# Performance work log

Measured on AMD Instinct MI355X. Metric: run time of the kernel, lower is better.

The kernel has to match this reference:

```python
import jax, jax.numpy as jnp
import numpy as np

BN_EPS = 1e-5


def lstm_scan(x, Wih, Whh, b):
    # x: [B, T, I] -> outputs [B, T, H]; PyTorch gate order i, f, g, o
    B = x.shape[0]
    H = Whh.shape[1]
    xs = jnp.swapaxes(x, 0, 1)  # [T, B, I]

    def step(carry, xt):
        h, c = carry
        z = xt @ Wih.T + h @ Whh.T + b  # [B, 4H]
        i, f, g, o = jnp.split(z, 4, axis=-1)
        c = jax.nn.sigmoid(f) * c + jax.nn.sigmoid(i) * jnp.tanh(g)
        h = jax.nn.sigmoid(o) * jnp.tanh(c)
        return (h, c), h

    init = (jnp.zeros((B, H), x.dtype), jnp.zeros((B, H), x.dtype))
    _, hs = jax.lax.scan(step, init, xs)
    return jnp.swapaxes(hs, 0, 1)


def bilstm(x, Wf, Uf, bf, Wr, Ur, br):
    fwd = lstm_scan(x, Wf, Uf, bf)
    rev = lstm_scan(x[:, ::-1], Wr, Ur, br)[:, ::-1]
    return jnp.concatenate([fwd, rev], axis=-1)


def batchnorm(x, g, b):
    # training-mode BN: batch mean, biased variance (PyTorch forward default)
    mu = x.mean(axis=0)
    var = x.var(axis=0)
    return g * (x - mu) * jax.lax.rsqrt(var + BN_EPS) + b


def setup_inputs() -> dict:
    key = jax.random.key(0)
    ks = jax.random.split(key, 20)
    B = 1048576
    idx = jax.random.randint(ks[0], (B, 1), 0, 8).astype(jnp.float32)
    feats = jax.random.normal(ks[1], (B, 7), dtype=jnp.float32)
    x = jnp.concatenate([idx, feats], axis=1)  # [B, 8]

    def p(k, shape):
        return 0.1 * jax.random.normal(k, shape, dtype=jnp.float32)

    return {
        "x": x,
        "emb": p(ks[2], (8, 2)),
        "W1": p(ks[3], (18, 9)), "b1": p(ks[4], (18,)),
        "g1": jnp.ones((18,), jnp.float32), "be1": jnp.zeros((18,), jnp.float32),
        "W2": p(ks[5], (9, 18)), "b2": p(ks[6], (9,)),
        "g2": jnp.ones((9,), jnp.float32), "be2": jnp.zeros((9,), jnp.float32),
        # lstm1: input 1, hidden 2, bidirectional
        "l1Wf": p(ks[7], (8, 1)), "l1Uf": p(ks[8], (8, 2)), "l1bf": p(ks[9], (8,)),
        "l1Wr": p(ks[10], (8, 1)), "l1Ur": p(ks[11], (8, 2)), "l1br": p(ks[12], (8,)),
        # lstm2: input 4, hidden 1, bidirectional
        "l2Wf": p(ks[13], (4, 4)), "l2Uf": p(ks[14], (4, 1)), "l2bf": p(ks[15], (4,)),
        "l2Wr": p(ks[16], (4, 4)), "l2Ur": p(ks[17], (4, 1)), "l2br": p(ks[18], (4,)),
    }


def reference(x, emb, W1, b1, g1, be1, W2, b2, g2, be2,
              l1Wf, l1Uf, l1bf, l1Wr, l1Ur, l1br,
              l2Wf, l2Uf, l2bf, l2Wr, l2Ur, l2br):
    idx = x[:, 0].astype(jnp.int32)
    e = emb[idx]                                   # [B, 2]
    h = jnp.concatenate([e, x[:, 1:]], axis=1)     # [B, 9]
    h = jax.nn.relu(batchnorm(h @ W1.T + b1, g1, be1))   # [B, 18]
    h = jax.nn.relu(batchnorm(h @ W2.T + b2, g2, be2))   # [B, 9]
    h = h[:, :, None]                              # [B, 9, 1]
    h = jax.nn.relu(bilstm(h, l1Wf, l1Uf, l1bf, l1Wr, l1Ur, l1br))  # [B, 9, 4]
    h = bilstm(h, l2Wf, l2Uf, l2bf, l2Wr, l2Ur, l2br)               # [B, 9, 2]
    return h.reshape(-1, 9, 2)
```

## Files before the change

kernel.cpp:

```cpp
#include <hip/hip_runtime.h>

#define LOG2E 1.4426950408889634f
#define BN_EPS 1e-5f

typedef float f32x2 __attribute__((ext_vector_type(2)));
typedef float f32x4 __attribute__((ext_vector_type(4)));

__device__ __forceinline__ float sigf(float x){
    return __builtin_amdgcn_rcpf(1.f + __builtin_amdgcn_exp2f(-LOG2E * x));
}
__device__ __forceinline__ float sigtanh(float a, float b){
    float A  = __builtin_amdgcn_exp2f(LOG2E * a);
    float Bv = __builtin_amdgcn_exp2f((2.f * LOG2E) * b);
    float num = A * (Bv - 1.f);
    float den = (1.f + A) * (1.f + Bv);
    return num * __builtin_amdgcn_rcpf(den);
}
__device__ __forceinline__ float relu_(float x){ return fmaxf(x, 0.f); }

__device__ __forceinline__ float wsum(float v){
    #pragma unroll
    for (int m = 32; m >= 1; m >>= 1) v += __shfl_xor(v, m, 64);
    return v;
}

__device__ constexpr int TRI(int j, int l){ return j*9 - j*(j-1)/2 + (l - j); }

__device__ __forceinline__ void load_h0(const float* __restrict__ x, const float* __restrict__ emb,
                                        long row, float h0[9])
{
    const float4* xv = (const float4*)(x + row * 8);
    float4 p = xv[0];
    float4 q = xv[1];
    int idx = (int)p.x;
    float2 e = ((const float2*)emb)[idx];
    h0[0] = e.x; h0[1] = e.y;
    h0[2] = p.y; h0[3] = p.z; h0[4] = p.w;
    h0[5] = q.x; h0[6] = q.y; h0[7] = q.z; h0[8] = q.w;
}

__global__ __launch_bounds__(256) void k_moments(const float* __restrict__ x, const float* __restrict__ emb,
                                                 float* __restrict__ stats, int B)
{
    float s9[9], mt[45];
    #pragma unroll
    for (int j = 0; j < 9; ++j) s9[j] = 0.f;
    #pragma unroll
    for (int t = 0; t < 45; ++t) mt[t] = 0.f;

    long base = (long)blockIdx.x * 1024 + threadIdx.x;
    #pragma unroll
    for (int r = 0; r < 4; ++r){
        long row = base + r * 256;
        if (row < B){
            float h0[9];
            load_h0(x, emb, row, h0);
            #pragma unroll
            for (int j = 0; j < 9; ++j){
                s9[j] += h0[j];
                #pragma unroll
                for (int l = j; l < 9; ++l)
                    mt[TRI(j,l)] = fmaf(h0[j], h0[l], mt[TRI(j,l)]);
            }
        }
    }
    __shared__ float sm[54];
    if (threadIdx.x < 54) sm[threadIdx.x] = 0.f;
    __syncthreads();
    bool l0 = (threadIdx.x & 63) == 0;
    #pragma unroll
    for (int j = 0; j < 9; ++j){
        float v = wsum(s9[j]);
        if (l0) atomicAdd(&sm[j], v);
    }
    #pragma unroll
    for (int t = 0; t < 45; ++t){
        float v = wsum(mt[t]);
        if (l0) atomicAdd(&sm[9 + t], v);
    }
    __syncthreads();
    if (threadIdx.x < 9)  atomicAdd(&stats[threadIdx.x], sm[threadIdx.x]);
    else if (threadIdx.x < 54) atomicAdd(&stats[16 + threadIdx.x - 9], sm[threadIdx.x]);
}

__device__ __forceinline__ void bn1_from_moments(const float* __restrict__ stats,
                                                 const float* __restrict__ W1, const float* __restrict__ b1,
                                                 const float* __restrict__ g1, const float* __restrict__ be1,
                                                 float invB, float* smem_sc, float* smem_sh)
{
    if (threadIdx.x < 18){
        int k = threadIdx.x;
        float w[9];
        #pragma unroll
        for (int j = 0; j < 9; ++j) w[j] = W1[k*9 + j];
        float dot9 = 0.f, q = 0.f;
        #pragma unroll
        for (int j = 0; j < 9; ++j){
            dot9 = fmaf(w[j], stats[j], dot9);
            q = fmaf(w[j]*w[j], stats[16 + TRI(j,j)], q);
            #pragma unroll
            for (int l = j+1; l < 9; ++l)
                q = fmaf(2.f*w[j]*w[l], stats[16 + TRI(j,l)], q);
        }
        float m1  = dot9 * invB;
        float var = fmaf(-m1, m1, q * invB);
        float mu  = m1 + b1[k];
        float sc  = g1[k] * __builtin_amdgcn_rsqf(var + BN_EPS);
        smem_sc[k] = sc;
        smem_sh[k] = fmaf(-mu, sc, be1[k]);
    }
    __syncthreads();
}

template<int STORE_Z2>
__global__ __launch_bounds__(256) void k_stats2(const float* __restrict__ x, const float* __restrict__ emb,
                                                const float* __restrict__ W1, const float* __restrict__ b1,
                                                const float* __restrict__ g1, const float* __restrict__ be1,
                                                const float* __restrict__ W2, const float* __restrict__ b2,
                                                float* __restrict__ stats, float* __restrict__ z2buf, int B)
{
    __shared__ float s_sc[18], s_sh[18];
    bn1_from_moments(stats, W1, b1, g1, be1, 1.f/(float)B, s_sc, s_sh);

    float sc1[18], sh1[18];
    #pragma unroll
    for (int k = 0; k < 18; ++k){ sc1[k] = s_sc[k]; sh1[k] = s_sh[k]; }

    float as[9], aq[9];
    #pragma unroll
    for (int k = 0; k < 9; ++k){ as[k] = 0.f; aq[k] = 0.f; }

    long base = (long)blockIdx.x * 1024 + threadIdx.x;
    #pragma unroll
    for (int r = 0; r < 4; ++r){
        long row = base + r * 256;
        if (row < B){
            float h0[9];
            load_h0(x, emb, row, h0);
            float a1[18];
            #pragma unroll
            for (int k = 0; k < 18; ++k){
                float s = b1[k];
                #pragma unroll
                for (int j = 0; j < 9; ++j) s = fmaf(W1[k*9 + j], h0[j], s);
                a1[k] = relu_(fmaf(sc1[k], s, sh1[k]));
            }
            #pragma unroll
            for (int k = 0; k < 9; ++k){
                float s = b2[k];
                #pragma unroll
                for (int j = 0; j < 18; ++j) s = fmaf(W2[k*18 + j], a1[j], s);
                as[k] += s; aq[k] = fmaf(s, s, aq[k]);
                if (STORE_Z2) z2buf[(long)k * B + row] = s;
            }
        }
    }
    __shared__ float sm[18];
    if (threadIdx.x < 18) sm[threadIdx.x] = 0.f;
    __syncthreads();
    bool l0 = (threadIdx.x & 63) == 0;
    #pragma unroll
    for (int k = 0; k < 9; ++k){
        float s = wsum(as[k]);
        float q = wsum(aq[k]);
        if (l0){ atomicAdd(&sm[k], s); atomicAdd(&sm[9 + k], q); }
    }
    __syncthreads();
    if (threadIdx.x < 9)       atomicAdd(&stats[64 + threadIdx.x], sm[threadIdx.x]);
    else if (threadIdx.x < 18) atomicAdd(&stats[80 + threadIdx.x - 9], sm[threadIdx.x]);
}

__device__ __forceinline__ f32x2 mk2(float a, float b){ f32x2 r; r.x=a; r.y=b; return r; }
__device__ __forceinline__ f32x4 mk4(float a, float b, float c, float d){ f32x4 r; r.x=a; r.y=b; r.z=c; r.w=d; return r; }

template<int USE_WS>
__global__ __launch_bounds__(256) void k_main(const float* __restrict__ x, const float* __restrict__ emb,
    const float* __restrict__ W1, const float* __restrict__ b1,
    const float* __restrict__ g1, const float* __restrict__ be1,
    const float* __restrict__ W2, const float* __restrict__ b2,
    const float* __restrict__ g2, const float* __restrict__ be2,
    const float* __restrict__ w1f, const float* __restrict__ u1f, const float* __restrict__ c1f,
    const float* __restrict__ w1r, const float* __restrict__ u1r, const float* __restrict__ c1r,
    const float* __restrict__ w2f, const float* __restrict__ u2f, const float* __restrict__ c2f,
    const float* __restrict__ w2r, const float* __restrict__ u2r, const float* __restrict__ c2r,
    const float* __restrict__ stats, const float* __restrict__ z2buf,
    float* __restrict__ out, int B)
{
    __shared__ float s_sc[18], s_sh[18];
    float invB = 1.f / (float)B;
    if (!USE_WS) bn1_from_moments(stats, W1, b1, g1, be1, invB, s_sc, s_sh);

    long row = (long)blockIdx.x * 256 + threadIdx.x;
    if (row >= B) return;

    float a2[9];
    #pragma unroll
    for (int k = 0; k < 9; ++k){
        float zc;
        if (USE_WS){
            zc = z2buf[(long)k * B + row];
        } else {
            zc = 0.f;
        }
        a2[k] = zc;
    }
    if (!USE_WS){
        float h0[9];
        load_h0(x, emb, row, h0);
        float a1[18];
        #pragma unroll
        for (int k = 0; k < 18; ++k){
            float s = b1[k];
            #pragma unroll
            for (int j = 0; j < 9; ++j) s = fmaf(W1[k*9 + j], h0[j], s);
            a1[k] = relu_(fmaf(s_sc[k], s, s_sh[k]));
        }
        #pragma unroll
        for (int k = 0; k < 9; ++k){
            float s = b2[k];
            #pragma unroll
            for (int j = 0; j < 18; ++j) s = fmaf(W2[k*18 + j], a1[j], s);
            a2[k] = s;
        }
    }
    #pragma unroll
    for (int k = 0; k < 9; ++k){
        float mu  = stats[64 + k] * invB;
        float var = fmaf(-mu, mu, stats[80 + k] * invB);
        float sc  = g2[k] * __builtin_amdgcn_rsqf(var + BN_EPS);
        a2[k] = relu_(fmaf(sc, a2[k] - mu, be2[k]));
    }

    f32x4 W4[4], U04[4], U14[4], B4[4];
    #pragma unroll
    for (int g = 0; g < 4; ++g){
        W4[g]  = mk4(w1f[2*g], w1f[2*g+1], w1r[2*g], w1r[2*g+1]);
        U04[g] = mk4(u1f[(2*g)*2], u1f[(2*g+1)*2], u1r[(2*g)*2], u1r[(2*g+1)*2]);
        U14[g] = mk4(u1f[(2*g)*2+1], u1f[(2*g+1)*2+1], u1r[(2*g)*2+1], u1r[(2*g+1)*2+1]);
        B4[g]  = mk4(c1f[2*g], c1f[2*g+1], c1r[2*g], c1r[2*g+1]);
    }
    f32x4 h4 = {0.f, 0.f, 0.f, 0.f};
    f32x4 c4 = {0.f, 0.f, 0.f, 0.f};
    float u_[9][4];
    #pragma unroll
    for (int s = 0; s < 9; ++s){
        const int tf = s, tr = 8 - s;
        f32x4 xt4 = mk4(a2[tf], a2[tf], a2[tr], a2[tr]);
        f32x4 hx  = mk4(h4.x, h4.x, h4.z, h4.z);
        f32x4 hy  = mk4(h4.y, h4.y, h4.w, h4.w);
        f32x4 z[4];
        #pragma unroll
        for (int g = 0; g < 4; ++g)
            z[g] = __builtin_elementwise_fma(W4[g], xt4,
                    __builtin_elementwise_fma(U04[g], hx,
                     __builtin_elementwise_fma(U14[g], hy, B4[g])));
        f32x4 icg, fs;
        #pragma unroll
        for (int c = 0; c < 4; ++c){
            icg[c] = sigtanh(z[0][c], z[2][c]);
            fs[c]  = sigf(z[1][c]);
        }
        c4 = __builtin_elementwise_fma(fs, c4, icg);
        #pragma unroll
        for (int c = 0; c < 4; ++c) h4[c] = sigtanh(z[3][c], c4[c]);
        u_[tf][0] = relu_(h4.x);
        u_[tf][1] = relu_(h4.y);
        u_[tr][2] = relu_(h4.z);
        u_[tr][3] = relu_(h4.w);
    }

    f32x2 w2v[4][4], u2v[4], b2v[4];
    #pragma unroll
    for (int r = 0; r < 4; ++r){
        #pragma unroll
        for (int j = 0; j < 4; ++j) w2v[r][j] = mk2(w2f[4*r + j], w2r[4*r + j]);
        u2v[r] = mk2(u2f[r], u2r[r]);
        b2v[r] = mk2(c2f[r], c2r[r]);
    }
    f32x2 h2 = {0.f, 0.f};
    f32x2 cc = {0.f, 0.f};
    long obase = row * 18;
    #pragma unroll
    for (int s = 0; s < 9; ++s){
        const int tf = s, tr = 8 - s;
        f32x2 z[4];
        #pragma unroll
        for (int r = 0; r < 4; ++r){
            f32x2 acc = __builtin_elementwise_fma(u2v[r], h2, b2v[r]);
            #pragma unroll
            for (int j = 0; j < 4; ++j)
                acc = __builtin_elementwise_fma(w2v[r][j], mk2(u_[tf][j], u_[tr][j]), acc);
            z[r] = acc;
        }
        f32x2 icg, fs;
        #pragma unroll
        for (int c = 0; c < 2; ++c){
            icg[c] = sigtanh(z[0][c], z[2][c]);
            fs[c]  = sigf(z[1][c]);
        }
        cc = __builtin_elementwise_fma(fs, cc, icg);
        float hfo = sigtanh(z[3][0], cc.x);
        float hro = sigtanh(z[3][1], cc.y);
        h2 = mk2(hfo, hro);
        out[obase + 2*tf]     = hfo;
        out[obase + 2*tr + 1] = hro;
    }
}

extern "C" void kernel_launch(void* const* d_in, const int* in_sizes, int n_in,
                              void* d_out, int out_size, void* d_ws, size_t ws_size,
                              hipStream_t stream)
{
    const float* x    = (const float*)d_in[0];
    const float* emb  = (const float*)d_in[1];
    const float* W1   = (const float*)d_in[2];
    const float* b1   = (const float*)d_in[3];
    const float* g1   = (const float*)d_in[4];
    const float* be1  = (const float*)d_in[5];
    const float* W2   = (const float*)d_in[6];
    const float* b2   = (const float*)d_in[7];
    const float* g2   = (const float*)d_in[8];
    const float* be2  = (const float*)d_in[9];
    const float* l1Wf = (const float*)d_in[10];
    const float* l1Uf = (const float*)d_in[11];
    const float* l1bf = (const float*)d_in[12];
    const float* l1Wr = (const float*)d_in[13];
    const float* l1Ur = (const float*)d_in[14];
    const float* l1br = (const float*)d_in[15];
    const float* l2Wf = (const float*)d_in[16];
    const float* l2Uf = (const float*)d_in[17];
    const float* l2bf = (const float*)d_in[18];
    const float* l2Wr = (const float*)d_in[19];
    const float* l2Ur = (const float*)d_in[20];
    const float* l2br = (const float*)d_in[21];

    int B = in_sizes[0] / 8;
    float* stats = (float*)d_ws;
    float* z2buf = (float*)d_ws + 1024;
    size_t need = (1024 + (size_t)9 * B) * sizeof(float);
    bool use_ws = ws_size >= need;

    hipMemsetAsync(d_ws, 0, 128 * sizeof(float), stream);

    int nb12 = (B + 1023) / 1024;
    int nb3  = (B + 255) / 256;

    k_moments<<<nb12, 256, 0, stream>>>(x, emb, stats, B);
    if (use_ws){
        k_stats2<1><<<nb12, 256, 0, stream>>>(x, emb, W1, b1, g1, be1, W2, b2, stats, z2buf, B);
        k_main<1><<<nb3, 256, 0, stream>>>(x, emb, W1, b1, g1, be1, W2, b2, g2, be2,
                                           l1Wf, l1Uf, l1bf, l1Wr, l1Ur, l1br,
                                           l2Wf, l2Uf, l2bf, l2Wr, l2Ur, l2br,
                                           stats, z2buf, (float*)d_out, B);
    } else {
        k_stats2<0><<<nb12, 256, 0, stream>>>(x, emb, W1, b1, g1, be1, W2, b2, stats, z2buf, B);
        k_main<0><<<nb3, 256, 0, stream>>>(x, emb, W1, b1, g1, be1, W2, b2, g2, be2,
                                           l1Wf, l1Uf, l1bf, l1Wr, l1Ur, l1br,
                                           l2Wf, l2Uf, l2bf, l2Wr, l2Ur, l2br,
                                           stats, z2buf, (float*)d_out, B);
    }
}
```

Measured before the change: 152.9 us.

## Fuse three passes into one cooperative kernel with grid syncs, keeping z2 in registers

Replaces the moments, stats2 and main kernels with a single cooperative kernel that uses grid.sync between the BN statistics phases. Each thread keeps its four rows' z2 values in registers, which removes the 9*B workspace write and re-read and the extra kernel launches. Outputs are staged and written as float2 pairs. The cost is that all 1024 blocks must be co-resident (launch_bounds 256,4), which means high register pressure and possible spills. If the occupancy check fails, the code falls back to a three-kernel path that recomputes z2.

```diff
diff --git a/kernel.cpp b/kernel.cpp
--- a/kernel.cpp
+++ b/kernel.cpp
@@ -1,4 +1,7 @@
 #include <hip/hip_runtime.h>
+#include <hip/hip_cooperative_groups.h>
+
+namespace cg = cooperative_groups;
 
 #define LOG2E 1.4426950408889634f
 #define BN_EPS 1e-5f
@@ -39,50 +42,6 @@
     h0[5] = q.x; h0[6] = q.y; h0[7] = q.z; h0[8] = q.w;
 }
 
-__global__ __launch_bounds__(256) void k_moments(const float* __restrict__ x, const float* __restrict__ emb,
-                                                 float* __restrict__ stats, int B)
-{
-    float s9[9], mt[45];
-    #pragma unroll
-    for (int j = 0; j < 9; ++j) s9[j] = 0.f;
-    #pragma unroll
-    for (int t = 0; t < 45; ++t) mt[t] = 0.f;
-
-    long base = (long)blockIdx.x * 1024 + threadIdx.x;
-    #pragma unroll
-    for (int r = 0; r < 4; ++r){
-        long row = base + r * 256;
-        if (row < B){
-            float h0[9];
-            load_h0(x, emb, row, h0);
-            #pragma unroll
-            for (int j = 0; j < 9; ++j){
-                s9[j] += h0[j];
-                #pragma unroll
-                for (int l = j; l < 9; ++l)
-                    mt[TRI(j,l)] = fmaf(h0[j], h0[l], mt[TRI(j,l)]);
-            }
-        }
-    }
-    __shared__ float sm[54];
-    if (threadIdx.x < 54) sm[threadIdx.x] = 0.f;
-    __syncthreads();
-    bool l0 = (threadIdx.x & 63) == 0;
-    #pragma unroll
-    for (int j = 0; j < 9; ++j){
-        float v = wsum(s9[j]);
-        if (l0) atomicAdd(&sm[j], v);
-    }
-    #pragma unroll
-    for (int t = 0; t < 45; ++t){
-        float v = wsum(mt[t]);
-        if (l0) atomicAdd(&sm[9 + t], v);
-    }
-    __syncthreads();
-    if (threadIdx.x < 9)  atomicAdd(&stats[threadIdx.x], sm[threadIdx.x]);
-    else if (threadIdx.x < 54) atomicAdd(&stats[16 + threadIdx.x - 9], sm[threadIdx.x]);
-}
-
 __device__ __forceinline__ void bn1_from_moments(const float* __restrict__ stats,
                                                  const float* __restrict__ W1, const float* __restrict__ b1,
                                                  const float* __restrict__ g1, const float* __restrict__ be1,
@@ -112,23 +71,233 @@
     __syncthreads();
 }
 
-template<int STORE_Z2>
-__global__ __launch_bounds__(256) void k_stats2(const float* __restrict__ x, const float* __restrict__ emb,
-                                                const float* __restrict__ W1, const float* __restrict__ b1,
-                                                const float* __restrict__ g1, const float* __restrict__ be1,
-                                                const float* __restrict__ W2, const float* __restrict__ b2,
-                                                float* __restrict__ stats, float* __restrict__ z2buf, int B)
-{
-    __shared__ float s_sc[18], s_sh[18];
-    bn1_from_moments(stats, W1, b1, g1, be1, 1.f/(float)B, s_sc, s_sh);
-
-    float sc1[18], sh1[18];
-    #pragma unroll
-    for (int k = 0; k < 18; ++k){ sc1[k] = s_sc[k]; sh1[k] = s_sh[k]; }
-
-    float as[9], aq[9];
-    #pragma unroll
-    for (int k = 0; k < 9; ++k){ as[k] = 0.f; aq[k] = 0.f; }
+__device__ __forceinline__ f32x2 mk2(float a, float b){ f32x2 r; r.x=a; r.y=b; return r; }
+__device__ __forceinline__ f32x4 mk4(float a, float b, float c, float d){ f32x4 r; r.x=a; r.y=b; r.z=c; r.w=d; return r; }
+
+struct KParams {
+    const float *x, *emb, *W1, *b1, *g1, *be1, *W2, *b2, *g2, *be2;
+    const float *w1f, *u1f, *c1f, *w1r, *u1r, *c1r;
+    const float *w2f, *u2f, *c2f, *w2r, *u2r, *c2r;
+    float* stats;
+    float* out;
+    int B;
+};
+
+__global__ __launch_bounds__(256, 4) void k_fused(KParams p)
+{
+    cg::grid_group grid = cg::this_grid();
+    const int tid = threadIdx.x;
+    const long base = (long)blockIdx.x * 1024 + tid;
+    const float invB = 1.f / (float)p.B;
+    const bool l0 = (tid & 63) == 0;
+
+    {
+        float s9[9], mt[45];
+        #pragma unroll
+        for (int j = 0; j < 9; ++j) s9[j] = 0.f;
+        #pragma unroll
+        for (int t = 0; t < 45; ++t) mt[t] = 0.f;
+
+        #pragma unroll
+        for (int r = 0; r < 4; ++r){
+            long row = base + r * 256;
+            if (row < p.B){
+                float h0[9];
+                load_h0(p.x, p.emb, row, h0);
+                #pragma unroll
+                for (int j = 0; j < 9; ++j){
+                    s9[j] += h0[j];
+                    #pragma unroll
+                    for (int l = j; l < 9; ++l)
+                        mt[TRI(j,l)] = fmaf(h0[j], h0[l], mt[TRI(j,l)]);
+                }
+            }
+        }
+        __shared__ float sm[54];
+        if (tid < 54) sm[tid] = 0.f;
+        __syncthreads();
+        #pragma unroll
+        for (int j = 0; j < 9; ++j){
+            float v = wsum(s9[j]);
+            if (l0) atomicAdd(&sm[j], v);
+        }
+        #pragma unroll
+        for (int t = 0; t < 45; ++t){
+            float v = wsum(mt[t]);
+            if (l0) atomicAdd(&sm[9 + t], v);
+        }
+        __syncthreads();
+        if (tid < 9)       atomicAdd(&p.stats[tid], sm[tid]);
+        else if (tid < 54) atomicAdd(&p.stats[16 + tid - 9], sm[tid]);
+    }
+
+    grid.sync();
+
+    float z2r[4][9];
+    {
+        __shared__ float s_sc[18], s_sh[18];
+        bn1_from_moments(p.stats, p.W1, p.b1, p.g1, p.be1, invB, s_sc, s_sh);
+
+        float sc1[18], sh1[18];
+        #pragma unroll
+        for (int k = 0; k < 18; ++k){ sc1[k] = s_sc[k]; sh1[k] = s_sh[k]; }
+
+        float as[9], aq[9];
+        #pragma unroll
+        for (int k = 0; k < 9; ++k){ as[k] = 0.f; aq[k] = 0.f; }
+
+        #pragma unroll
+        for (int r = 0; r < 4; ++r){
+            long row = base + r * 256;
+            if (row < p.B){
+                float h0[9];
+                load_h0(p.x, p.emb, row, h0);
+                float a1[18];
+                #pragma unroll
+                for (int k = 0; k < 18; ++k){
+                    float s = p.b1[k];
+                    #pragma unroll
+                    for (int j = 0; j < 9; ++j) s = fmaf(p.W1[k*9 + j], h0[j], s);
+                    a1[k] = relu_(fmaf(sc1[k], s, sh1[k]));
+                }
+                #pragma unroll
+                for (int k = 0; k < 9; ++k){
+                    float s = p.b2[k];
+                    #pragma unroll
+                    for (int j = 0; j < 18; ++j) s = fmaf(p.W2[k*18 + j], a1[j], s);
+                    z2r[r][k] = s;
+                    as[k] += s; aq[k] = fmaf(s, s, aq[k]);
+                }
+            } else {
+                #pragma unroll
+                for (int k = 0; k < 9; ++k) z2r[r][k] = 0.f;
+            }
+        }
+        __shared__ float sm2[18];
+        if (tid < 18) sm2[tid] = 0.f;
+        __syncthreads();
+        #pragma unroll
+        for (int k = 0; k < 9; ++k){
+            float s = wsum(as[k]);
+            float q = wsum(aq[k]);
+            if (l0){ atomicAdd(&sm2[k], s); atomicAdd(&sm2[9 + k], q); }
+        }
+        __syncthreads();
+        if (tid < 9)       atomicAdd(&p.stats[64 + tid], sm2[tid]);
+        else if (tid < 18) atomicAdd(&p.stats[80 + tid - 9], sm2[tid]);
+    }
+
+    grid.sync();
+
+    float sc2[9], sh2[9];
+    #pragma unroll
+    for (int k = 0; k < 9; ++k){
+        float mu  = p.stats[64 + k] * invB;
+        float var = fmaf(-mu, mu, p.stats[80 + k] * invB);
+        float sc  = p.g2[k] * __builtin_amdgcn_rsqf(var + BN_EPS);
+        sc2[k] = sc;
+        sh2[k] = fmaf(-mu, sc, p.be2[k]);
+    }
+
+    f32x4 W4[4], U04[4], U14[4], B4[4];
+    #pragma unroll
+    for (int g = 0; g < 4; ++g){
+        W4[g]  = mk4(p.w1f[2*g], p.w1f[2*g+1], p.w1r[2*g], p.w1r[2*g+1]);
+        U04[g] = mk4(p.u1f[(2*g)*2], p.u1f[(2*g+1)*2], p.u1r[(2*g)*2], p.u1r[(2*g+1)*2]);
+        U14[g] = mk4(p.u1f[(2*g)*2+1], p.u1f[(2*g+1)*2+1], p.u1r[(2*g)*2+1], p.u1r[(2*g+1)*2+1]);
+        B4[g]  = mk4(p.c1f[2*g], p.c1f[2*g+1], p.c1r[2*g], p.c1r[2*g+1]);
+    }
+    f32x2 w2v[4][4], u2v[4], b2v[4];
+    #pragma unroll
+    for (int r = 0; r < 4; ++r){
+        #pragma unroll
+        for (int j = 0; j < 4; ++j) w2v[r][j] = mk2(p.w2f[4*r + j], p.w2r[4*r + j]);
+        u2v[r] = mk2(p.u2f[r], p.u2r[r]);
+        b2v[r] = mk2(p.c2f[r], p.c2r[r]);
+    }
+
+    #pragma unroll
+    for (int r = 0; r < 4; ++r){
+        long row = base + r * 256;
+        if (row >= p.B) continue;
+
+        float a2[9];
+        #pragma unroll
+        for (int k = 0; k < 9; ++k)
+            a2[k] = relu_(fmaf(sc2[k], z2r[r][k], sh2[k]));
+
+        f32x4 h4 = {0.f, 0.f, 0.f, 0.f};
+        f32x4 c4 = {0.f, 0.f, 0.f, 0.f};
+        float u_[9][4];
+        #pragma unroll
+        for (int s = 0; s < 9; ++s){
+            const int tf = s, tr = 8 - s;
+            f32x4 xt4 = mk4(a2[tf], a2[tf], a2[tr], a2[tr]);
+            f32x4 hx  = mk4(h4.x, h4.x, h4.z, h4.z);
+            f32x4 hy  = mk4(h4.y, h4.y, h4.w, h4.w);
+            f32x4 z[4];
+            #pragma unroll
+            for (int g = 0; g < 4; ++g)
+                z[g] = __builtin_elementwise_fma(W4[g], xt4,
+                        __builtin_elementwise_fma(U04[g], hx,
+                         __builtin_elementwise_fma(U14[g], hy, B4[g])));
+            f32x4 icg, fs;
+            #pragma unroll
+            for (int c = 0; c < 4; ++c){
+                icg[c] = sigtanh(z[0][c], z[2][c]);
+                fs[c]  = sigf(z[1][c]);
+            }
+            c4 = __builtin_elementwise_fma(fs, c4, icg);
+            #pragma unroll
+            for (int c = 0; c < 4; ++c) h4[c] = sigtanh(z[3][c], c4[c]);
+            u_[tf][0] = relu_(h4.x);
+            u_[tf][1] = relu_(h4.y);
+            u_[tr][2] = relu_(h4.z);
+            u_[tr][3] = relu_(h4.w);
+        }
+
+        f32x2 h2 = {0.f, 0.f};
+        f32x2 cc = {0.f, 0.f};
+        float of[9], orr[9];
+        #pragma unroll
+        for (int s = 0; s < 9; ++s){
+            const int tf = s, tr = 8 - s;
+            f32x2 z[4];
+            #pragma unroll
+            for (int g = 0; g < 4; ++g){
+                f32x2 acc = __builtin_elementwise_fma(u2v[g], h2, b2v[g]);
+                #pragma unroll
+                for (int j = 0; j < 4; ++j)
+                    acc = __builtin_elementwise_fma(w2v[g][j], mk2(u_[tf][j], u_[tr][j]), acc);
+                z[g] = acc;
+            }
+            f32x2 icg, fs;
+            #pragma unroll
+            for (int c = 0; c < 2; ++c){
+                icg[c] = sigtanh(z[0][c], z[2][c]);
+                fs[c]  = sigf(z[1][c]);
+            }
+            cc = __builtin_elementwise_fma(fs, cc, icg);
+            float hfo = sigtanh(z[3][0], cc.x);
+            float hro = sigtanh(z[3][1], cc.y);
+            h2 = mk2(hfo, hro);
+            of[tf]  = hfo;
+            orr[tr] = hro;
+        }
+        float2* op = (float2*)(p.out + row * 18);
+        #pragma unroll
+        for (int t = 0; t < 9; ++t) op[t] = make_float2(of[t], orr[t]);
+    }
+}
+
+__global__ __launch_bounds__(256) void k_moments(const float* __restrict__ x, const float* __restrict__ emb,
+                                                 float* __restrict__ stats, int B)
+{
+    float s9[9], mt[45];
+    #pragma unroll
+    for (int j = 0; j < 9; ++j) s9[j] = 0.f;
+    #pragma unroll
+    for (int t = 0; t < 45; ++t) mt[t] = 0.f;
 
     long base = (long)blockIdx.x * 1024 + threadIdx.x;
     #pragma unroll
@@ -137,21 +306,68 @@
         if (row < B){
             float h0[9];
             load_h0(x, emb, row, h0);
+            #pragma unroll
+            for (int j = 0; j < 9; ++j){
+                s9[j] += h0[j];
+                #pragma unroll
+                for (int l = j; l < 9; ++l)
+                    mt[TRI(j,l)] = fmaf(h0[j], h0[l], mt[TRI(j,l)]);
+            }
+        }
+    }
+    __shared__ float sm[54];
+    if (threadIdx.x < 54) sm[threadIdx.x] = 0.f;
+    __syncthreads();
+    bool l0 = (threadIdx.x & 63) == 0;
+    #pragma unroll
+    for (int j = 0; j < 9; ++j){
+        float v = wsum(s9[j]);
+        if (l0) atomicAdd(&sm[j], v);
+    }
+    #pragma unroll
+    for (int t = 0; t < 45; ++t){
+        float v = wsum(mt[t]);
+        if (l0) atomicAdd(&sm[9 + t], v);
+    }
+    __syncthreads();
+    if (threadIdx.x < 9)  atomicAdd(&stats[threadIdx.x], sm[threadIdx.x]);
+    else if (threadIdx.x < 54) atomicAdd(&stats[16 + threadIdx.x - 9], sm[threadIdx.x]);
+}
+
+__global__ __launch_bounds__(256) void k_stats2(KParams p)
+{
+    __shared__ float s_sc[18], s_sh[18];
+    bn1_from_moments(p.stats, p.W1, p.b1, p.g1, p.be1, 1.f/(float)p.B, s_sc, s_sh);
+
+    float sc1[18], sh1[18];
+    #pragma unroll
+    for (int k = 0; k < 18; ++k){ sc1[k] = s_sc[k]; sh1[k] = s_sh[k]; }
+
+    float as[9], aq[9];
+    #pragma unroll
+    for (int k = 0; k < 9; ++k){ as[k] = 0.f; aq[k] = 0.f; }
+
+    long base = (long)blockIdx.x * 1024 + threadIdx.x;
+    #pragma unroll
+    for (int r = 0; r < 4; ++r){
+        long row = base + r * 256;
+        if (row < p.B){
+            float h0[9];
+            load_h0(p.x, p.emb, row, h0);
             float a1[18];
             #pragma unroll
             for (int k = 0; k < 18; ++k){
-                float s = b1[k];
-                #pragma unroll
-                for (int j = 0; j < 9; ++j) s = fmaf(W1[k*9 + j], h0[j], s);
+                float s = p.b1[k];
+                #pragma unroll
+                for (int j = 0; j < 9; ++j) s = fmaf(p.W1[k*9 + j], h0[j], s);
                 a1[k] = relu_(fmaf(sc1[k], s, sh1[k]));
             }
             #pragma unroll
             for (int k = 0; k < 9; ++k){
-                float s = b2[k];
-                #pragma unroll
-                for (int j = 0; j < 18; ++j) s = fmaf(W2[k*18 + j], a1[j], s);
+                float s = p.b2[k];
+                #pragma unroll
+                for (int j = 0; j < 18; ++j) s = fmaf(p.W2[k*18 + j], a1[j], s);
                 as[k] += s; aq[k] = fmaf(s, s, aq[k]);
-                if (STORE_Z2) z2buf[(long)k * B + row] = s;
             }
         }
     }
@@ -166,78 +382,48 @@
         if (l0){ atomicAdd(&sm[k], s); atomicAdd(&sm[9 + k], q); }
     }
     __syncthreads();
-    if (threadIdx.x < 9)       atomicAdd(&stats[64 + threadIdx.x], sm[threadIdx.x]);
-    else if (threadIdx.x < 18) atomicAdd(&stats[80 + threadIdx.x - 9], sm[threadIdx.x]);
-}
-
-__device__ __forceinline__ f32x2 mk2(float a, float b){ f32x2 r; r.x=a; r.y=b; return r; }
-__device__ __forceinline__ f32x4 mk4(float a, float b, float c, float d){ f32x4 r; r.x=a; r.y=b; r.z=c; r.w=d; return r; }
-
-template<int USE_WS>
-__global__ __launch_bounds__(256) void k_main(const float* __restrict__ x, const float* __restrict__ emb,
-    const float* __restrict__ W1, const float* __restrict__ b1,
-    const float* __restrict__ g1, const float* __restrict__ be1,
-    const float* __restrict__ W2, const float* __restrict__ b2,
-    const float* __restrict__ g2, const float* __restrict__ be2,
-    const float* __restrict__ w1f, const float* __restrict__ u1f, const float* __restrict__ c1f,
-    const float* __restrict__ w1r, const float* __restrict__ u1r, const float* __restrict__ c1r,
-    const float* __restrict__ w2f, const float* __restrict__ u2f, const float* __restrict__ c2f,
-    const float* __restrict__ w2r, const float* __restrict__ u2r, const float* __restrict__ c2r,
-    const float* __restrict__ stats, const float* __restrict__ z2buf,
-    float* __restrict__ out, int B)
+    if (threadIdx.x < 9)       atomicAdd(&p.stats[64 + threadIdx.x], sm[threadIdx.x]);
+    else if (threadIdx.x < 18) atomicAdd(&p.stats[80 + threadIdx.x - 9], sm[threadIdx.x]);
+}
+
+__global__ __launch_bounds__(256) void k_main_fb(KParams p)
 {
     __shared__ float s_sc[18], s_sh[18];
-    float invB = 1.f / (float)B;
-    if (!USE_WS) bn1_from_moments(stats, W1, b1, g1, be1, invB, s_sc, s_sh);
+    float invB = 1.f / (float)p.B;
+    bn1_from_moments(p.stats, p.W1, p.b1, p.g1, p.be1, invB, s_sc, s_sh);
 
     long row = (long)blockIdx.x * 256 + threadIdx.x;
-    if (row >= B) return;
-
+    if (row >= p.B) return;
+
+    float h0[9];
+    load_h0(p.x, p.emb, row, h0);
+    float a1[18];
+    #pragma unroll
+    for (int k = 0; k < 18; ++k){
+        float s = p.b1[k];
+        #pragma unroll
+        for (int j = 0; j < 9; ++j) s = fmaf(p.W1[k*9 + j], h0[j], s);
+        a1[k] = relu_(fmaf(s_sc[k], s, s_sh[k]));
+    }
     float a2[9];
     #pragma unroll
     for (int k = 0; k < 9; ++k){
-        float zc;
-        if (USE_WS){
-            zc = z2buf[(long)k * B + row];
-        } else {
-            zc = 0.f;
-        }
-        a2[k] = zc;
-    }
-    if (!USE_WS){
-        float h0[9];
-        load_h0(x, emb, row, h0);
-        float a1[18];
-        #pragma unroll
-        for (int k = 0; k < 18; ++k){
-            float s = b1[k];
-            #pragma unroll
-            for (int j = 0; j < 9; ++j) s = fmaf(W1[k*9 + j], h0[j], s);
-            a1[k] = relu_(fmaf(s_sc[k], s, s_sh[k]));
-        }
-        #pragma unroll
-        for (int k = 0; k < 9; ++k){
-            float s = b2[k];
-            #pragma unroll
-            for (int j = 0; j < 18; ++j) s = fmaf(W2[k*18 + j], a1[j], s);
-            a2[k] = s;
-        }
-    }
-    #pragma unroll
-    for (int k = 0; k < 9; ++k){
-        float mu  = stats[64 + k] * invB;
-        float var = fmaf(-mu, mu, stats[80 + k] * invB);
-        float sc  = g2[k] * __builtin_amdgcn_rsqf(var + BN_EPS);
-        a2[k] = relu_(fmaf(sc, a2[k] - mu, be2[k]));
+        float s = p.b2[k];
+        #pragma unroll
+        for (int j = 0; j < 18; ++j) s = fmaf(p.W2[k*18 + j], a1[j], s);
+        float mu  = p.stats[64 + k] * invB;
+        float var = fmaf(-mu, mu, p.stats[80 + k] * invB);
+        float sc  = p.g2[k] * __builtin_amdgcn_rsqf(var + BN_EPS);
+        a2[k] = relu_(fmaf(sc, s - mu, p.be2[k]));
     }
 
     f32x4 W4[4], U04[4], U14[4], B4[4];
     #pragma unroll
     for (int g = 0; g < 4; ++g){
-        W4[g]  = mk4(w1f[2*g], w1f[2*g+1], w1r[2*g], w1r[2*g+1]);
-        U04[g] = mk4(u1f[(2*g)*2], u1f[(2*g+1)*2], u1r[(2*g)*2], u1r[(2*g+1)*2]);
-        U14[g] = mk4(u1f[(2*g)*2+1], u1f[(2*g+1)*2+1], u1r[(2*g)*2+1], u1r[(2*g+1)*2+1]);
-        B4[g]  = mk4(c1f[2*g], c1f[2*g+1], c1r[2*g], c1r[2*g+1]);
+        W4[g]  = mk4(p.w1f[2*g], p.w1f[2*g+1], p.w1r[2*g], p.w1r[2*g+1]);
+        U04[g] = mk4(p.u1f[(2*g)*2], p.u1f[(2*g+1)*2], p.u1r[(2*g)*2], p.u1r[(2*g+1)*2]);
+        U14[g] = mk4(p.u1f[(2*g)*2+1], p.u1f[(2*g+1)*2+1], p.u1r[(2*g)*2+1], p.u1r[(2*g+1)*2+1]);
+        B4[g]  = mk4(p.c1f[2*g], p.c1f[2*g+1], p.c1r[2*g], p.c1r[2*g+1]);
     }
     f32x4 h4 = {0.f, 0.f, 0.f, 0.f};
     f32x4 c4 = {0.f, 0.f, 0.f, 0.f};
@@ -273,24 +459,24 @@
     #pragma unroll
     for (int r = 0; r < 4; ++r){
         #pragma unroll
-        for (int j = 0; j < 4; ++j) w2v[r][j] = mk2(w2f[4*r + j], w2r[4*r + j]);
-        u2v[r] = mk2(u2f[r], u2r[r]);
-        b2v[r] = mk2(c2f[r], c2r[r]);
+        for (int j = 0; j < 4; ++j) w2v[r][j] = mk2(p.w2f[4*r + j], p.w2r[4*r + j]);
+        u2v[r] = mk2(p.u2f[r], p.u2r[r]);
+        b2v[r] = mk2(p.c2f[r], p.c2r[r]);
     }
     f32x2 h2 = {0.f, 0.f};
     f32x2 cc = {0.f, 0.f};
-    long obase = row * 18;
+    float of[9], orr[9];
     #pragma unroll
     for (int s = 0; s < 9; ++s){
         const int tf = s, tr = 8 - s;
         f32x2 z[4];
         #pragma unroll
-        for (int r = 0; r < 4; ++r){
-            f32x2 acc = __builtin_elementwise_fma(u2v[r], h2, b2v[r]);
+        for (int g = 0; g < 4; ++g){
+            f32x2 acc = __builtin_elementwise_fma(u2v[g], h2, b2v[g]);
             #pragma unroll
             for (int j = 0; j < 4; ++j)
-                acc = __builtin_elementwise_fma(w2v[r][j], mk2(u_[tf][j], u_[tr][j]), acc);
-            z[r] = acc;
+                acc = __builtin_elementwise_fma(w2v[g][j], mk2(u_[tf][j], u_[tr][j]), acc);
+            z[g] = acc;
         }
         f32x2 icg, fs;
         #pragma unroll
@@ -302,61 +488,66 @@
         float hfo = sigtanh(z[3][0], cc.x);
         float hro = sigtanh(z[3][1], cc.y);
         h2 = mk2(hfo, hro);
-        out[obase + 2*tf]     = hfo;
-        out[obase + 2*tr + 1] = hro;
-    }
+        of[tf]  = hfo;
+        orr[tr] = hro;
+    }
+    float2* op = (float2*)(p.out + row * 18);
+    #pragma unroll
+    for (int t = 0; t < 9; ++t) op[t] = make_float2(of[t], orr[t]);
 }
 
 extern "C" void kernel_launch(void* const* d_in, const int* in_sizes, int n_in,
                               void* d_out, int out_size, void* d_ws, size_t ws_size,
                               hipStream_t stream)
 {
-    const float* x    = (const float*)d_in[0];
-    const float* emb  = (const float*)d_in[1];
-    const float* W1   = (const float*)d_in[2];
-    const float* b1   = (const float*)d_in[3];
-    const float* g1   = (const float*)d_in[4];
-    const float* be1  = (const float*)d_in[5];
-    const float* W2   = (const float*)d_in[6];
-    const float* b2   = (const float*)d_in[7];
-    const float* g2   = (const float*)d_in[8];
-    const float* be2  = (const float*)d_in[9];
-    const float* l1Wf = (const float*)d_in[10];
-    const float* l1Uf = (const float*)d_in[11];
-    const float* l1bf = (const float*)d_in[12];
-    const float* l1Wr = (const float*)d_in[13];
-    const float* l1Ur = (const float*)d_in[14];
-    const float* l1br = (const float*)d_in[15];
-    const float* l2Wf = (const float*)d_in[16];
-    const float* l2Uf = (const float*)d_in[17];
-    const float* l2bf = (const float*)d_in[18];
-    const float* l2Wr = (const float*)d_in[19];
-    const float* l2Ur = (const float*)d_in[20];
-    const float* l2br = (const float*)d_in[21];
-
-    int B = in_sizes[0] / 8;
-    float* stats = (float*)d_ws;
-    float* z2buf = (float*)d_ws + 1024;
-    size_t need = (1024 + (size_t)9 * B) * sizeof(float);
-    bool use_ws = ws_size >= need;
+    KParams p;
+    p.x    = (const float*)d_in[0];
+    p.emb  = (const float*)d_in[1];
+    p.W1   = (const float*)d_in[2];
+    p.b1   = (const float*)d_in[3];
+    p.g1   = (const float*)d_in[4];
+    p.be1  = (const float*)d_in[5];
+    p.W2   = (const float*)d_in[6];
+    p.b2   = (const float*)d_in[7];
+    p.g2   = (const float*)d_in[8];
+    p.be2  = (const float*)d_in[9];
+    p.w1f  = (const float*)d_in[10];
+    p.u1f  = (const float*)d_in[11];
+    p.c1f  = (const float*)d_in[12];
+    p.w1r  = (const float*)d_in[13];
+    p.u1r  = (const float*)d_in[14];
+    p.c1r  = (const float*)d_in[15];
+    p.w2f  = (const float*)d_in[16];
+    p.u2f  = (const float*)d_in[17];
+    p.c2f  = (const float*)d_in[18];
+    p.w2r  = (const float*)d_in[19];
+    p.u2r  = (const float*)d_in[20];
+    p.c2r  = (const float*)d_in[21];
+    p.stats = (float*)d_ws;
+    p.out   = (float*)d_out;
+    p.B     = in_sizes[0] / 8;
 
     hipMemsetAsync(d_ws, 0, 128 * sizeof(float), stream);
 
-    int nb12 = (B + 1023) / 1024;
-    int nb3  = (B + 255) / 256;
-
-    k_moments<<<nb12, 256, 0, stream>>>(x, emb, stats, B);
-    if (use_ws){
-        k_stats2<1><<<nb12, 256, 0, stream>>>(x, emb, W1, b1, g1, be1, W2, b2, stats, z2buf, B);
-        k_main<1><<<nb3, 256, 0, stream>>>(x, emb, W1, b1, g1, be1, W2, b2, g2, be2,
-                                           l1Wf, l1Uf, l1bf, l1Wr, l1Ur, l1br,
-                                           l2Wf, l2Uf, l2bf, l2Wr, l2Ur, l2br,
-                                           stats, z2buf, (float*)d_out, B);
-    } else {
-        k_stats2<0><<<nb12, 256, 0, stream>>>(x, emb, W1, b1, g1, be1, W2, b2, stats, z2buf, B);
-        k_main<0><<<nb3, 256, 0, stream>>>(x, emb, W1, b1, g1, be1, W2, b2, g2, be2,
-                                           l1Wf, l1Uf, l1bf, l1Wr, l1Ur, l1br,
-                                           l2Wf, l2Uf, l2bf, l2Wr, l2Ur, l2br,
-                                           stats, z2buf, (float*)d_out, B);
-    }
-}
+    int nb = (p.B + 1023) / 1024;
+
+    bool coop_done = false;
+    int dev = 0;
+    hipGetDevice(&dev);
+    int cus = 0;
+    hipDeviceGetAttribute(&cus, hipDeviceAttributeMultiprocessorCount, dev);
+    int maxb = 0;
+    hipError_t oe = hipOccupancyMaxActiveBlocksPerMultiprocessor(&maxb, k_fused, 256, 0);
+    if (oe == hipSuccess && cus > 0 && (long)maxb * cus >= nb){
+        void* args[] = { (void*)&p };
+        hipError_t e = hipLaunchCooperativeKernel((void*)k_fused, dim3(nb), dim3(256), args, 0, stream);
+        coop_done = (e == hipSuccess);
+    }
+
+    if (!coop_done){
+        int nb3 = (p.B + 255) / 256;
+        k_moments<<<nb, 256, 0, stream>>>(p.x, p.emb, p.stats, p.B);
+        k_stats2<<<nb, 256, 0, stream>>>(p);
+        k_main_fb<<<nb3, 256, 0, stream>>>(p);
+    }
+}
```

New measurement: 155.4 us. No clear change (+1.6%).

## Process two rows per thread with packed f32x2 math across rows

Applied to the files above, without the earlier changes.

The main kernel now has each thread handle two batch rows (rA and rA+256) and packs the two rows into f32x2 lanes. Before, the forward and reverse directions were packed into f32x4. All LSTM gate FMAs and activations run on these two-row vectors, so uniform weights broadcast as scalars and packed FMA can be used. The grid is halved. This raises per-thread ILP and amortizes weight loads, but increases register pressure and reduces the number of waves in flight.

```diff
diff --git a/kernel.cpp b/kernel.cpp
--- a/kernel.cpp
+++ b/kernel.cpp
@@ -4,18 +4,7 @@
 #define BN_EPS 1e-5f
 
 typedef float f32x2 __attribute__((ext_vector_type(2)));
-typedef float f32x4 __attribute__((ext_vector_type(4)));
-
-__device__ __forceinline__ float sigf(float x){
-    return __builtin_amdgcn_rcpf(1.f + __builtin_amdgcn_exp2f(-LOG2E * x));
-}
-__device__ __forceinline__ float sigtanh(float a, float b){
-    float A  = __builtin_amdgcn_exp2f(LOG2E * a);
-    float Bv = __builtin_amdgcn_exp2f((2.f * LOG2E) * b);
-    float num = A * (Bv - 1.f);
-    float den = (1.f + A) * (1.f + Bv);
-    return num * __builtin_amdgcn_rcpf(den);
-}
+
 __device__ __forceinline__ float relu_(float x){ return fmaxf(x, 0.f); }
 
 __device__ __forceinline__ float wsum(float v){
@@ -171,10 +160,34 @@
 }
 
 __device__ __forceinline__ f32x2 mk2(float a, float b){ f32x2 r; r.x=a; r.y=b; return r; }
-__device__ __forceinline__ f32x4 mk4(float a, float b, float c, float d){ f32x4 r; r.x=a; r.y=b; r.z=c; r.w=d; return r; }
+__device__ __forceinline__ f32x2 sp2(float a){ f32x2 r; r.x=a; r.y=a; return r; }
+__device__ __forceinline__ f32x2 exp2v(f32x2 v){
+    f32x2 r; r.x = __builtin_amdgcn_exp2f(v.x); r.y = __builtin_amdgcn_exp2f(v.y); return r;
+}
+__device__ __forceinline__ f32x2 rcpv(f32x2 v){
+    f32x2 r; r.x = __builtin_amdgcn_rcpf(v.x); r.y = __builtin_amdgcn_rcpf(v.y); return r;
+}
+__device__ __forceinline__ f32x2 relu2(f32x2 v){
+    f32x2 r; r.x = fmaxf(v.x, 0.f); r.y = fmaxf(v.y, 0.f); return r;
+}
+__device__ __forceinline__ f32x2 fmas(float a, f32x2 b, f32x2 c){
+    return __builtin_elementwise_fma(sp2(a), b, c);
+}
+
+__device__ __forceinline__ f32x2 cellh2(f32x2 zi, f32x2 zf, f32x2 zg, f32x2 zo, f32x2& c){
+    f32x2 A  = exp2v(sp2(LOG2E) * zi);
+    f32x2 G  = exp2v(sp2(2.f*LOG2E) * zg);
+    f32x2 icg = A * (G - sp2(1.f)) * rcpv((sp2(1.f) + A) * (sp2(1.f) + G));
+    f32x2 Fp = exp2v(sp2(-LOG2E) * zf);
+    f32x2 fs = rcpv(sp2(1.f) + Fp);
+    c = __builtin_elementwise_fma(fs, c, icg);
+    f32x2 O  = exp2v(sp2(LOG2E) * zo);
+    f32x2 T  = exp2v(sp2(2.f*LOG2E) * c);
+    return O * (T - sp2(1.f)) * rcpv((sp2(1.f) + O) * (sp2(1.f) + T));
+}
 
 template<int USE_WS>
-__global__ __launch_bounds__(256) void k_main(const float* __restrict__ x, const float* __restrict__ emb,
+__global__ __launch_bounds__(256) void k_main2(const float* __restrict__ x, const float* __restrict__ emb,
     const float* __restrict__ W1, const float* __restrict__ b1,
     const float* __restrict__ g1, const float* __restrict__ be1,
     const float* __restrict__ W2, const float* __restrict__ b2,
@@ -190,120 +203,115 @@
     float invB = 1.f / (float)B;
     if (!USE_WS) bn1_from_moments(stats, W1, b1, g1, be1, invB, s_sc, s_sh);
 
-    long row = (long)blockIdx.x * 256 + threadIdx.x;
-    if (row >= B) return;
-
-    float a2[9];
-    #pragma unroll
-    for (int k = 0; k < 9; ++k){
-        float zc;
-        if (USE_WS){
-            zc = z2buf[(long)k * B + row];
-        } else {
-            zc = 0.f;
-        }
-        a2[k] = zc;
-    }
-    if (!USE_WS){
-        float h0[9];
-        load_h0(x, emb, row, h0);
-        float a1[18];
-        #pragma unroll
-        for (int k = 0; k < 18; ++k){
-            float s = b1[k];
-            #pragma unroll
-            for (int j = 0; j < 9; ++j) s = fmaf(W1[k*9 + j], h0[j], s);
-            a1[k] = relu_(fmaf(s_sc[k], s, s_sh[k]));
-        }
+    long rA = (long)blockIdx.x * 512 + threadIdx.x;
+    long rB = rA + 256;
+    if (rA >= B) return;
+    bool vB = rB < B;
+    long rBl = vB ? rB : rA;
+
+    f32x2 a2[9];
+    if (USE_WS){
         #pragma unroll
         for (int k = 0; k < 9; ++k){
-            float s = b2[k];
-            #pragma unroll
-            for (int j = 0; j < 18; ++j) s = fmaf(W2[k*18 + j], a1[j], s);
-            a2[k] = s;
-        }
+            float zA = z2buf[(long)k * B + rA];
+            float zBv = z2buf[(long)k * B + rBl];
+            a2[k] = mk2(zA, zBv);
+        }
+    } else {
+        float zz[2][9];
+        #pragma unroll
+        for (int rr = 0; rr < 2; ++rr){
+            long row = rr ? rBl : rA;
+            float h0[9];
+            load_h0(x, emb, row, h0);
+            float a1[18];
+            #pragma unroll
+            for (int k = 0; k < 18; ++k){
+                float s = b1[k];
+                #pragma unroll
+                for (int j = 0; j < 9; ++j) s = fmaf(W1[k*9 + j], h0[j], s);
+                a1[k] = relu_(fmaf(s_sc[k], s, s_sh[k]));
+            }
+            #pragma unroll
+            for (int k = 0; k < 9; ++k){
+                float s = b2[k];
+                #pragma unroll
+                for (int j = 0; j < 18; ++j) s = fmaf(W2[k*18 + j], a1[j], s);
+                zz[rr][k] = s;
+            }
+        }
+        #pragma unroll
+        for (int k = 0; k < 9; ++k) a2[k] = mk2(zz[0][k], zz[1][k]);
     }
     #pragma unroll
     for (int k = 0; k < 9; ++k){
         float mu  = stats[64 + k] * invB;
         float var = fmaf(-mu, mu, stats[80 + k] * invB);
         float sc  = g2[k] * __builtin_amdgcn_rsqf(var + BN_EPS);
-        a2[k] = relu_(fmaf(sc, a2[k] - mu, be2[k]));
-    }
-
-    f32x4 W4[4], U04[4], U14[4], B4[4];
-    #pragma unroll
-    for (int g = 0; g < 4; ++g){
-        W4[g]  = mk4(w1f[2*g], w1f[2*g+1], w1r[2*g], w1r[2*g+1]);
-        U04[g] = mk4(u1f[(2*g)*2], u1f[(2*g+1)*2], u1r[(2*g)*2], u1r[(2*g+1)*2]);
-        U14[g] = mk4(u1f[(2*g)*2+1], u1f[(2*g+1)*2+1], u1r[(2*g)*2+1], u1r[(2*g+1)*2+1]);
-        B4[g]  = mk4(c1f[2*g], c1f[2*g+1], c1r[2*g], c1r[2*g+1]);
-    }
-    f32x4 h4 = {0.f, 0.f, 0.f, 0.f};
-    f32x4 c4 = {0.f, 0.f, 0.f, 0.f};
-    float u_[9][4];
+        float sh  = fmaf(-mu, sc, be2[k]);
+        a2[k] = relu2(fmas(sc, a2[k], sp2(sh)));
+    }
+
+    f32x2 hf0 = sp2(0.f), hf1 = sp2(0.f), cf0 = sp2(0.f), cf1 = sp2(0.f);
+    f32x2 hr0 = sp2(0.f), hr1 = sp2(0.f), cr0 = sp2(0.f), cr1 = sp2(0.f);
+    f32x2 uu[9][4];
     #pragma unroll
     for (int s = 0; s < 9; ++s){
         const int tf = s, tr = 8 - s;
-        f32x4 xt4 = mk4(a2[tf], a2[tf], a2[tr], a2[tr]);
-        f32x4 hx  = mk4(h4.x, h4.x, h4.z, h4.z);
-        f32x4 hy  = mk4(h4.y, h4.y, h4.w, h4.w);
-        f32x4 z[4];
-        #pragma unroll
-        for (int g = 0; g < 4; ++g)
-            z[g] = __builtin_elementwise_fma(W4[g], xt4,
-                    __builtin_elementwise_fma(U04[g], hx,
-                     __builtin_elementwise_fma(U14[g], hy, B4[g])));
-        f32x4 icg, fs;
-        #pragma unroll
-        for (int c = 0; c < 4; ++c){
-            icg[c] = sigtanh(z[0][c], z[2][c]);
-            fs[c]  = sigf(z[1][c]);
-        }
-        c4 = __builtin_elementwise_fma(fs, c4, icg);
-        #pragma unroll
-        for (int c = 0; c < 4; ++c) h4[c] = sigtanh(z[3][c], c4[c]);
-        u_[tf][0] = relu_(h4.x);
-        u_[tf][1] = relu_(h4.y);
-        u_[tr][2] = relu_(h4.z);
-        u_[tr][3] = relu_(h4.w);
-    }
-
-    f32x2 w2v[4][4], u2v[4], b2v[4];
-    #pragma unroll
-    for (int r = 0; r < 4; ++r){
-        #pragma unroll
-        for (int j = 0; j < 4; ++j) w2v[r][j] = mk2(w2f[4*r + j], w2r[4*r + j]);
-        u2v[r] = mk2(u2f[r], u2r[r]);
-        b2v[r] = mk2(c2f[r], c2r[r]);
-    }
-    f32x2 h2 = {0.f, 0.f};
-    f32x2 cc = {0.f, 0.f};
-    long obase = row * 18;
+        f32x2 xf = a2[tf], xr = a2[tr];
+        {
+            f32x2 zi0 = fmas(w1f[0], xf, fmas(u1f[0],  hf0, fmas(u1f[1],  hf1, sp2(c1f[0]))));
+            f32x2 zi1 = fmas(w1f[1], xf, fmas(u1f[2],  hf0, fmas(u1f[3],  hf1, sp2(c1f[1]))));
+            f32x2 zf0 = fmas(w1f[2], xf, fmas(u1f[4],  hf0, fmas(u1f[5],  hf1, sp2(c1f[2]))));
+            f32x2 zf1 = fmas(w1f[3], xf, fmas(u1f[6],  hf0, fmas(u1f[7],  hf1, sp2(c1f[3]))));
+            f32x2 zg0 = fmas(w1f[4], xf, fmas(u1f[8],  hf0, fmas(u1f[9],  hf1, sp2(c1f[4]))));
+            f32x2 zg1 = fmas(w1f[5], xf, fmas(u1f[10], hf0, fmas(u1f[11], hf1, sp2(c1f[5]))));
+            f32x2 zo0 = fmas(w1f[6], xf, fmas(u1f[12], hf0, fmas(u1f[13], hf1, sp2(c1f[6]))));
+            f32x2 zo1 = fmas(w1f[7], xf, fmas(u1f[14], hf0, fmas(u1f[15], hf1, sp2(c1f[7]))));
+            hf0 = cellh2(zi0, zf0, zg0, zo0, cf0);
+            hf1 = cellh2(zi1, zf1, zg1, zo1, cf1);
+        }
+        {
+            f32x2 zi0 = fmas(w1r[0], xr, fmas(u1r[0],  hr0, fmas(u1r[1],  hr1, sp2(c1r[0]))));
+            f32x2 zi1 = fmas(w1r[1], xr, fmas(u1r[2],  hr0, fmas(u1r[3],  hr1, sp2(c1r[1]))));
+            f32x2 zf0 = fmas(w1r[2], xr, fmas(u1r[4],  hr0, fmas(u1r[5],  hr1, sp2(c1r[2]))));
+            f32x2 zf1 = fmas(w1r[3], xr, fmas(u1r[6],  hr0, fmas(u1r[7],  hr1, sp2(c1r[3]))));
+            f32x2 zg0 = fmas(w1r[4], xr, fmas(u1r[8],  hr0, fmas(u1r[9],  hr1, sp2(c1r[4]))));
+            f32x2 zg1 = fmas(w1r[5], xr, fmas(u1r[10], hr0, fmas(u1r[11], hr1, sp2(c1r[5]))));
+            f32x2 zo0 = fmas(w1r[6], xr, fmas(u1r[12], hr0, fmas(u1r[13], hr1, sp2(c1r[6]))));
+            f32x2 zo1 = fmas(w1r[7], xr, fmas(u1r[14], hr0, fmas(u1r[15], hr1, sp2(c1r[7]))));
+            hr0 = cellh2(zi0, zf0, zg0, zo0, cr0);
+            hr1 = cellh2(zi1, zf1, zg1, zo1, cr1);
+        }
+        uu[tf][0] = relu2(hf0);
+        uu[tf][1] = relu2(hf1);
+        uu[tr][2] = relu2(hr0);
+        uu[tr][3] = relu2(hr1);
+    }
+
+    f32x2 H2f = sp2(0.f), C2fs = sp2(0.f), H2r = sp2(0.f), C2rs = sp2(0.f);
+    long oA = rA * 18, oB = rB * 18;
     #pragma unroll
     for (int s = 0; s < 9; ++s){
         const int tf = s, tr = 8 - s;
-        f32x2 z[4];
-        #pragma unroll
-        for (int r = 0; r < 4; ++r){
-            f32x2 acc = __builtin_elementwise_fma(u2v[r], h2, b2v[r]);
-            #pragma unroll
-            for (int j = 0; j < 4; ++j)
-                acc = __builtin_elementwise_fma(w2v[r][j], mk2(u_[tf][j], u_[tr][j]), acc);
-            z[r] = acc;
-        }
-        f32x2 icg, fs;
-        #pragma unroll
-        for (int c = 0; c < 2; ++c){
-            icg[c] = sigtanh(z[0][c], z[2][c]);
-            fs[c]  = sigf(z[1][c]);
-        }
-        cc = __builtin_elementwise_fma(fs, cc, icg);
-        float hfo = sigtanh(z[3][0], cc.x);
-        float hro = sigtanh(z[3][1], cc.y);
-        h2 = mk2(hfo, hro);
-        out[obase + 2*tf]     = hfo;
-        out[obase + 2*tr + 1] = hro;
+        {
+            f32x2 zi = fmas(w2f[0],  uu[tf][0], fmas(w2f[1],  uu[tf][1], fmas(w2f[2],  uu[tf][2], fmas(w2f[3],  uu[tf][3], fmas(u2f[0], H2f, sp2(c2f[0]))))));
+            f32x2 zf = fmas(w2f[4],  uu[tf][0], fmas(w2f[5],  uu[tf][1], fmas(w2f[6],  uu[tf][2], fmas(w2f[7],  uu[tf][3], fmas(u2f[1], H2f, sp2(c2f[1]))))));
+            f32x2 zg = fmas(w2f[8],  uu[tf][0], fmas(w2f[9],  uu[tf][1], fmas(w2f[10], uu[tf][2], fmas(w2f[11], uu[tf][3], fmas(u2f[2], H2f, sp2(c2f[2]))))));
+            f32x2 zo = fmas(w2f[12], uu[tf][0], fmas(w2f[13], uu[tf][1], fmas(w2f[14], uu[tf][2], fmas(w2f[15], uu[tf][3], fmas(u2f[3], H2f, sp2(c2f[3]))))));
+            H2f = cellh2(zi, zf, zg, zo, C2fs);
+            out[oA + 2*tf] = H2f.x;
+            if (vB) out[oB + 2*tf] = H2f.y;
+        }
+        {
+            f32x2 zi = fmas(w2r[0],  uu[tr][0], fmas(w2r[1],  uu[tr][1], fmas(w2r[2],  uu[tr][2], fmas(w2r[3],  uu[tr][3], fmas(u2r[0], H2r, sp2(c2r[0]))))));
+            f32x2 zf = fmas(w2r[4],  uu[tr][0], fmas(w2r[5],  uu[tr][1], fmas(w2r[6],  uu[tr][2], fmas(w2r[7],  uu[tr][3], fmas(u2r[1], H2r, sp2(c2r[1]))))));
+            f32x2 zg = fmas(w2r[8],  uu[tr][0], fmas(w2r[9],  uu[tr][1], fmas(w2r[10], uu[tr][2], fmas(w2r[11], uu[tr][3], fmas(u2r[2], H2r, sp2(c2r[2]))))));
+            f32x2 zo = fmas(w2r[12], uu[tr][0], fmas(w2r[13], uu[tr][1], fmas(w2r[14], uu[tr][2], fmas(w2r[15], uu[tr][3], fmas(u2r[3], H2r, sp2(c2r[3]))))));
+            H2r = cellh2(zi, zf, zg, zo, C2rs);
+            out[oA + 2*tr + 1] = H2r.x;
+            if (vB) out[oB + 2*tr + 1] = H2r.y;
+        }
     }
 }
 
@@ -343,20 +351,20 @@
     hipMemsetAsync(d_ws, 0, 128 * sizeof(float), stream);
 
     int nb12 = (B + 1023) / 1024;
-    int nb3  = (B + 255) / 256;
+    int nb3  = (B + 511) / 512;
 
     k_moments<<<nb12, 256, 0, stream>>>(x, emb, stats, B);
     if (use_ws){
         k_stats2<1><<<nb12, 256, 0, stream>>>(x, emb, W1, b1, g1, be1, W2, b2, stats, z2buf, B);
-        k_main<1><<<nb3, 256, 0, stream>>>(x, emb, W1, b1, g1, be1, W2, b2, g2, be2,
-                                           l1Wf, l1Uf, l1bf, l1Wr, l1Ur, l1br,
-                                           l2Wf, l2Uf, l2bf, l2Wr, l2Ur, l2br,
-                                           stats, z2buf, (float*)d_out, B);
+        k_main2<1><<<nb3, 256, 0, stream>>>(x, emb, W1, b1, g1, be1, W2, b2, g2, be2,
+                                            l1Wf, l1Uf, l1bf, l1Wr, l1Ur, l1br,
+                                            l2Wf, l2Uf, l2bf, l2Wr, l2Ur, l2br,
+                                            stats, z2buf, (float*)d_out, B);
     } else {
         k_stats2<0><<<nb12, 256, 0, stream>>>(x, emb, W1, b1, g1, be1, W2, b2, stats, z2buf, B);
-        k_main<0><<<nb3, 256, 0, stream>>>(x, emb, W1, b1, g1, be1, W2, b2, g2, be2,
-                                           l1Wf, l1Uf, l1bf, l1Wr, l1Ur, l1br,
-                                           l2Wf, l2Uf, l2bf, l2Wr, l2Ur, l2br,
-                                           stats, z2buf, (float*)d_out, B);
-    }
-}
+        k_main2<0><<<nb3, 256, 0, stream>>>(x, emb, W1, b1, g1, be1, W2, b2, g2, be2,
+                                            l1Wf, l1Uf, l1bf, l1Wr, l1Ur, l1br,
+                                            l2Wf, l2Uf, l2bf, l2Wr, l2Ur, l2br,
+                                            stats, z2buf, (float*)d_out, B);
+    }
+}
```

Measured after the change: 184.9 us. 20.9% more time.
